# Kernel optimization log

Measured on AMD Instinct MI355X. Metric: run time of the kernel, lower is better.

Reference implementation:

```python
import jax, jax.numpy as jnp
import numpy as np

B, N, CIN, H, W = 4, 1024, 256, 256, 256
R, C = 32, 32            # N = R*C table grid cells
PH, PW, SR = 3, 3, 2     # pool_size, sampling_ratio
D = 512                  # out_channels
SCALE = 0.25             # spatial_scale: image coords -> feature coords
IMG = 1024.0             # image size (H/SCALE)


def setup_inputs() -> dict:
    key = jax.random.key(0)
    ks = jax.random.split(key, 12)
    feats = jax.random.normal(ks[0], (B, CIN, H, W), jnp.float32)
    # build valid quadrilateral boxes (axis-aligned rectangles as 8-pt polys)
    x1 = jax.random.uniform(ks[1], (B, N), minval=0.0, maxval=IMG - 130.0)
    y1 = jax.random.uniform(ks[2], (B, N), minval=0.0, maxval=IMG - 130.0)
    bw = jax.random.uniform(ks[3], (B, N), minval=16.0, maxval=128.0)
    bh = jax.random.uniform(ks[4], (B, N), minval=16.0, maxval=128.0)
    x2, y2 = x1 + bw, y1 + bh
    boxes = jnp.stack([x1, y1, x2, y1, x2, y2, x1, y2], axis=-1)  # [B,N,8]
    img_sizes = jnp.full((B, 2), IMG, jnp.float32)
    IN = CIN * PH * PW
    W1 = jax.random.normal(ks[5], (IN, D), jnp.float32) * 0.02
    b1 = jnp.zeros((D,), jnp.float32)
    W2 = jax.random.normal(ks[6], (D, D), jnp.float32) * 0.02
    b2 = jnp.zeros((D,), jnp.float32)
    Wb = jax.random.normal(ks[7], (4, D), jnp.float32) * 0.02
    bb = jnp.zeros((D,), jnp.float32)
    g1 = jnp.ones((D,), jnp.float32); be1 = jnp.zeros((D,), jnp.float32)
    g2 = jnp.ones((D,), jnp.float32); be2 = jnp.zeros((D,), jnp.float32)
    return {"feats": feats, "boxes": boxes, "img_sizes": img_sizes,
            "W1": W1, "b1": b1, "W2": W2, "b2": b2, "Wb": Wb, "bb": bb,
            "g1": g1, "be1": be1, "g2": g2, "be2": be2}


def _layer_norm(x, g, b, eps=1e-5):
    mu = jnp.mean(x, axis=-1, keepdims=True)
    var = jnp.mean(jnp.square(x - mu), axis=-1, keepdims=True)
    return (x - mu) * jax.lax.rsqrt(var + eps) * g + b


def _bilinear(img, ys, xs):
    # img [Cin,H,W]; ys,xs [P] -> [Cin,P]; torchvision roi_align semantics:
    # zero outside (-1, dim); clamp into [0, dim-1] before interpolation.
    h, w = img.shape[1], img.shape[2]
    valid = (ys > -1.0) & (ys < h) & (xs > -1.0) & (xs < w)
    y = jnp.clip(ys, 0.0, h - 1.0)
    x = jnp.clip(xs, 0.0, w - 1.0)
    y0 = jnp.floor(y).astype(jnp.int32); x0 = jnp.floor(x).astype(jnp.int32)
    y1 = jnp.minimum(y0 + 1, h - 1);     x1 = jnp.minimum(x0 + 1, w - 1)
    ly = y - y0; lx = x - x0; hy = 1.0 - ly; hx = 1.0 - lx
    v = (img[:, y0, x0] * (hy * hx) + img[:, y0, x1] * (hy * lx)
         + img[:, y1, x0] * (ly * hx) + img[:, y1, x1] * (ly * lx))
    return v * valid


def _roi_align_one(img, bb):
    # img [Cin,H,W]; bb [N,4] already in feature coords -> [N,Cin,PH,PW]
    x1, y1, x2, y2 = bb[:, 0], bb[:, 1], bb[:, 2], bb[:, 3]
    rw = jnp.maximum(x2 - x1, 1.0); rh = jnp.maximum(y2 - y1, 1.0)
    binw = rw / PW; binh = rh / PH
    off = (jnp.arange(SR, dtype=jnp.float32) + 0.5) / SR
    gy = (jnp.arange(PH, dtype=jnp.float32)[:, None] + off[None, :]).reshape(-1)  # [PH*SR]
    gx = (jnp.arange(PW, dtype=jnp.float32)[:, None] + off[None, :]).reshape(-1)  # [PW*SR]
    ys = y1[:, None] + gy[None, :] * binh[:, None]  # [N,PH*SR]
    xs = x1[:, None] + gx[None, :] * binw[:, None]  # [N,PW*SR]
    YY = jnp.broadcast_to(ys[:, :, None], (bb.shape[0], PH * SR, PW * SR)).reshape(-1)
    XX = jnp.broadcast_to(xs[:, None, :], (bb.shape[0], PH * SR, PW * SR)).reshape(-1)
    vals = _bilinear(img, YY, XX)  # [Cin, N*PH*SR*PW*SR]
    vals = vals.reshape(CIN, bb.shape[0], PH, SR, PW, SR).mean(axis=(3, 5))
    return vals.transpose(1, 0, 2, 3)


def reference(feats, boxes, img_sizes, W1, b1, W2, b2, Wb, bb, g1, be1, g2, be2):
    # poly2bbox: [B,N,8] -> [B,N,4] axis-aligned boxes
    px, py = boxes[..., 0::2], boxes[..., 1::2]
    bbox = jnp.stack([px.min(-1), py.min(-1), px.max(-1), py.max(-1)], axis=-1)
    # rotated/regular RoIAlign (here bbox path), vmapped over batch images
    pooled = jax.vmap(_roi_align_one)(feats, bbox * SCALE)     # [B,N,Cin,PH,PW]
    flat = pooled.reshape(B, N, CIN * PH * PW)
    lines_feat = jax.nn.relu(flat @ W1 + b1) @ W2 + b2          # [B,N,D]
    # bbox positional embedding (coords normalized by image size)
    denom = jnp.concatenate([img_sizes, img_sizes], axis=-1)[:, None, :]  # [B,1,4] (w,h,w,h)
    pos = _layer_norm(bbox / denom @ Wb + bb, g1, be1)
    out = _layer_norm(lines_feat + pos, g2, be2)                # [B,N,D]
    # align_cells_feat: pack cells into grid [B,D,R,C] (uniform grid -> no pad)
    aligned = out.transpose(0, 2, 1).reshape(B, D, R, C)
    masks = jnp.ones((B, R, C), jnp.float32)
    return aligned, masks
```

## Files before the change

kernel.cpp:

```cpp
#include <hip/hip_runtime.h>
#include <hip/hip_bf16.h>
#include <cstdint>
#include <cstddef>

#define B_    4
#define N_    1024
#define CIN_  256
#define HW_   256
#define D_    512
#define INK_  2304
#define BN_   4096

typedef __attribute__((ext_vector_type(8))) short bf16x8;
typedef __attribute__((ext_vector_type(4))) float f32x4;
typedef __attribute__((ext_vector_type(4))) unsigned short us4;

#define AS1(p) ((const __attribute__((address_space(1))) void*)(p))
#define AS3(p) ((__attribute__((address_space(3))) void*)(p))

__device__ __forceinline__ unsigned short f2bf(float f) {
    union { float f; unsigned u; } v; v.f = f;
    unsigned r = v.u + 0x7fffu + ((v.u >> 16) & 1u);
    return (unsigned short)(r >> 16);
}

template <typename OutT>
__global__ __launch_bounds__(256) void k_t64(
    const float* __restrict__ src, OutT* __restrict__ dst,
    int Mrows, int Ncols, size_t sBatch, size_t dBatch)
{
    constexpr int PAD = (sizeof(OutT) == 2) ? 66 : 67;
    __shared__ OutT tile[64][PAD];
    const int n0 = blockIdx.x * 64;
    const int m0 = blockIdx.y * 64;
    const float* s = src + (size_t)blockIdx.z * sBatch;
    OutT* d = dst + (size_t)blockIdx.z * dBatch;
    const int t  = threadIdx.x;
    const int rr = t >> 4;
    const int cc = t & 15;

    #pragma unroll
    for (int i = 0; i < 4; ++i) {
        int row = i * 16 + rr;
        float4 v = *(const float4*)(s + (size_t)(m0 + row) * Ncols + n0 + cc * 4);
        if constexpr (sizeof(OutT) == 2) {
            tile[row][cc * 4 + 0] = f2bf(v.x);
            tile[row][cc * 4 + 1] = f2bf(v.y);
            tile[row][cc * 4 + 2] = f2bf(v.z);
            tile[row][cc * 4 + 3] = f2bf(v.w);
        } else {
            tile[row][cc * 4 + 0] = v.x;
            tile[row][cc * 4 + 1] = v.y;
            tile[row][cc * 4 + 2] = v.z;
            tile[row][cc * 4 + 3] = v.w;
        }
    }
    __syncthreads();
    #pragma unroll
    for (int i = 0; i < 4; ++i) {
        int p = i * 16 + rr;
        OutT v0 = tile[cc * 4 + 0][p];
        OutT v1 = tile[cc * 4 + 1][p];
        OutT v2 = tile[cc * 4 + 2][p];
        OutT v3 = tile[cc * 4 + 3][p];
        OutT* dp = d + (size_t)(n0 + p) * Mrows + m0 + cc * 4;
        if constexpr (sizeof(OutT) == 2) {
            *(us4*)dp = (us4){(unsigned short)v0, (unsigned short)v1,
                              (unsigned short)v2, (unsigned short)v3};
        } else {
            *(float4*)dp = make_float4(v0, v1, v2, v3);
        }
    }
}

__global__ __launch_bounds__(256) void k_roi3(
    const unsigned short* __restrict__ featsT, const float* __restrict__ boxes,
    unsigned short* __restrict__ flat)
{
    __shared__ int   so[4][36][4];
    __shared__ float sw[4][36][4];
    const int t = threadIdx.x;

    if (t < 144) {
        const int mbx = t / 36, s = t - mbx * 36;
        const int mbn = blockIdx.x * 4 + mbx;
        const float* bx = boxes + (size_t)mbn * 8;
        float xmn = fminf(fminf(bx[0], bx[2]), fminf(bx[4], bx[6]));
        float xmx = fmaxf(fmaxf(bx[0], bx[2]), fmaxf(bx[4], bx[6]));
        float ymn = fminf(fminf(bx[1], bx[3]), fminf(bx[5], bx[7]));
        float ymx = fmaxf(fmaxf(bx[1], bx[3]), fmaxf(bx[5], bx[7]));
        float sx1 = xmn * 0.25f, sy1 = ymn * 0.25f;
        float sx2 = xmx * 0.25f, sy2 = ymx * 0.25f;
        float rw = fmaxf(sx2 - sx1, 1.0f), rh = fmaxf(sy2 - sy1, 1.0f);
        float binw = rw * (1.0f / 3.0f), binh = rh * (1.0f / 3.0f);
        int row = s / 6, col = s % 6;
        float y = sy1 + (row * 0.5f + 0.25f) * binh;
        float x = sx1 + (col * 0.5f + 0.25f) * binw;
        float valid = (y > -1.0f && y < 256.0f && x > -1.0f && x < 256.0f) ? 1.0f : 0.0f;
        y = fminf(fmaxf(y, 0.0f), 255.0f);
        x = fminf(fmaxf(x, 0.0f), 255.0f);
        int y0 = (int)floorf(y), x0 = (int)floorf(x);
        int y1 = min(y0 + 1, 255), x1 = min(x0 + 1, 255);
        float ly = y - (float)y0, lx = x - (float)x0;
        float hy = 1.0f - ly, hx = 1.0f - lx;
        float m = 0.25f * valid;
        so[mbx][s][0] = y0 * HW_ + x0;  so[mbx][s][1] = y0 * HW_ + x1;
        so[mbx][s][2] = y1 * HW_ + x0;  so[mbx][s][3] = y1 * HW_ + x1;
        sw[mbx][s][0] = hy * hx * m;    sw[mbx][s][1] = hy * lx * m;
        sw[mbx][s][2] = ly * hx * m;    sw[mbx][s][3] = ly * lx * m;
    }
    __syncthreads();

    const int bxi = t >> 6;
    const int tid = t & 63;
    const int bn  = blockIdx.x * 4 + bxi;
    const int b   = bn >> 10;
    const uint2* basep = (const uint2*)featsT + (size_t)b * (65536ull * 64ull) + tid;

    float a0[9] = {0,0,0,0,0,0,0,0,0};
    float a1[9] = {0,0,0,0,0,0,0,0,0};
    float a2[9] = {0,0,0,0,0,0,0,0,0};
    float a3[9] = {0,0,0,0,0,0,0,0,0};
    #pragma unroll
    for (int j = 0; j < 36; ++j) {
        const int bin = ((j / 6) >> 1) * 3 + ((j % 6) >> 1);
        #pragma unroll
        for (int p = 0; p < 4; ++p) {
            float wgt = sw[bxi][j][p];
            uint2 u = basep[(size_t)so[bxi][j][p] << 6];
            a0[bin] += wgt * __uint_as_float(u.x << 16);
            a1[bin] += wgt * __uint_as_float(u.x & 0xffff0000u);
            a2[bin] += wgt * __uint_as_float(u.y << 16);
            a3[bin] += wgt * __uint_as_float(u.y & 0xffff0000u);
        }
    }

    unsigned short tmp[36];
    #pragma unroll
    for (int k = 0; k < 9; ++k) {
        tmp[k] = f2bf(a0[k]); tmp[9 + k] = f2bf(a1[k]);
        tmp[18 + k] = f2bf(a2[k]); tmp[27 + k] = f2bf(a3[k]);
    }
    unsigned* dst = (unsigned*)(flat + (size_t)bn * INK_ + tid * 36);
    #pragma unroll
    for (int k = 0; k < 18; ++k)
        dst[k] = (unsigned)tmp[2 * k] | ((unsigned)tmp[2 * k + 1] << 16);
}

template <int K, bool RELU_BF16OUT>
__global__ __launch_bounds__(256) void k_gemmB(
    const unsigned short* __restrict__ A,
    const unsigned short* __restrict__ Bt,
    const float* __restrict__ bias,
    unsigned short* __restrict__ Cbf,
    float* __restrict__ Cf)
{
    __shared__ __align__(16) unsigned short As[2][128 * 32];
    __shared__ __align__(16) unsigned short Bs[2][64 * 32];

    const int t = threadIdx.x;
    const int w = t >> 6;
    const int lane = t & 63;
    const int lane16 = lane & 15;
    const int q = lane >> 4;
    const int m0 = blockIdx.x * 128;
    const int n0 = blockIdx.y * 64;

    const int r4 = lane >> 2, c4 = lane & 3;
    const unsigned short* gA0 = A + (size_t)(m0 + w * 16 + r4) * K + c4 * 8;
    const unsigned short* gA1 = gA0 + (size_t)64 * K;
    const unsigned short* gB  = Bt + (size_t)(n0 + w * 16 + r4) * K + c4 * 8;

    f32x4 acc[2][4] = {};

    __builtin_amdgcn_global_load_lds(AS1(gA0), AS3(&As[0][(w * 16) * 32]), 16, 0, 0);
    __builtin_amdgcn_global_load_lds(AS1(gA1), AS3(&As[0][(64 + w * 16) * 32]), 16, 0, 0);
    __builtin_amdgcn_global_load_lds(AS1(gB ), AS3(&Bs[0][(w * 16) * 32]), 16, 0, 0);
    gA0 += 32; gA1 += 32; gB += 32;

    int cur = 0;
    for (int k0 = 0; k0 < K; k0 += 32) {
        __syncthreads();
        if (k0 + 32 < K) {
            __builtin_amdgcn_global_load_lds(AS1(gA0), AS3(&As[cur ^ 1][(w * 16) * 32]), 16, 0, 0);
            __builtin_amdgcn_global_load_lds(AS1(gA1), AS3(&As[cur ^ 1][(64 + w * 16) * 32]), 16, 0, 0);
            __builtin_amdgcn_global_load_lds(AS1(gB ), AS3(&Bs[cur ^ 1][(w * 16) * 32]), 16, 0, 0);
            gA0 += 32; gA1 += 32; gB += 32;
        }
        bf16x8 a0 = *(const bf16x8*)&As[cur][(w * 32 + lane16) * 32 + q * 8];
        bf16x8 a1 = *(const bf16x8*)&As[cur][(w * 32 + 16 + lane16) * 32 + q * 8];
        #pragma unroll
        for (int nt = 0; nt < 4; ++nt) {
            bf16x8 bv = *(const bf16x8*)&Bs[cur][(nt * 16 + lane16) * 32 + q * 8];
            acc[0][nt] = __builtin_amdgcn_mfma_f32_16x16x32_bf16(a0, bv, acc[0][nt], 0, 0, 0);
            acc[1][nt] = __builtin_amdgcn_mfma_f32_16x16x32_bf16(a1, bv, acc[1][nt], 0, 0, 0);
        }
        cur ^= 1;
    }

    #pragma unroll
    for (int nt = 0; nt < 4; ++nt) {
        int col = n0 + nt * 16 + lane16;
        float bs = bias[col];
        #pragma unroll
        for (int mg = 0; mg < 2; ++mg) {
            #pragma unroll
            for (int r = 0; r < 4; ++r) {
                int row = m0 + w * 32 + mg * 16 + q * 4 + r;
                float v = acc[mg][nt][r] + bs;
                if constexpr (RELU_BF16OUT) {
                    v = fmaxf(v, 0.0f);
                    Cbf[(size_t)row * D_ + col] = f2bf(v);
                } else {
                    Cf[(size_t)row * D_ + col] = v;
                }
            }
        }
    }
}

__global__ __launch_bounds__(256) void k_convert(
    const float* __restrict__ W1, const float* __restrict__ W2,
    unsigned short* __restrict__ W1t, unsigned short* __restrict__ W2t)
{
    int i = blockIdx.x * 256 + threadIdx.x;
    const int n1 = INK_ * D_;
    if (i < n1) {
        int n = i / INK_, k = i % INK_;
        W1t[i] = f2bf(W1[(size_t)k * D_ + n]);
    } else {
        int j = i - n1;
        if (j < D_ * D_) {
            int n = j / D_, k = j % D_;
            W2t[j] = f2bf(W2[(size_t)k * D_ + n]);
        }
    }
}

__global__ __launch_bounds__(256) void k_roi(
    const float* __restrict__ feats, const float* __restrict__ boxes,
    unsigned short* __restrict__ flat)
{
    __shared__ int   so[36][4];
    __shared__ float sw[36][4];
    const int bn = blockIdx.x;
    const int b  = bn >> 10;
    const int t  = threadIdx.x;

    if (t < 36) {
        const float* bx = boxes + (size_t)bn * 8;
        float xmn = fminf(fminf(bx[0], bx[2]), fminf(bx[4], bx[6]));
        float xmx = fmaxf(fmaxf(bx[0], bx[2]), fmaxf(bx[4], bx[6]));
        float ymn = fminf(fminf(bx[1], bx[3]), fminf(bx[5], bx[7]));
        float ymx = fmaxf(fmaxf(bx[1], bx[3]), fmaxf(bx[5], bx[7]));
        float sx1 = xmn * 0.25f, sy1 = ymn * 0.25f;
        float sx2 = xmx * 0.25f, sy2 = ymx * 0.25f;
        float rw = fmaxf(sx2 - sx1, 1.0f), rh = fmaxf(sy2 - sy1, 1.0f);
        float binw = rw * (1.0f / 3.0f), binh = rh * (1.0f / 3.0f);
        int row = t / 6, col = t % 6;
        float y = sy1 + (row * 0.5f + 0.25f) * binh;
        float x = sx1 + (col * 0.5f + 0.25f) * binw;
        float valid = (y > -1.0f && y < 256.0f && x > -1.0f && x < 256.0f) ? 1.0f : 0.0f;
        y = fminf(fmaxf(y, 0.0f), 255.0f);
        x = fminf(fmaxf(x, 0.0f), 255.0f);
        int y0 = (int)floorf(y), x0 = (int)floorf(x);
        int y1 = min(y0 + 1, 255), x1 = min(x0 + 1, 255);
        float ly = y - (float)y0, lx = x - (float)x0;
        float hy = 1.0f - ly, hx = 1.0f - lx;
        float m = 0.25f * valid;
        so[t][0] = y0 * HW_ + x0;  so[t][1] = y0 * HW_ + x1;
        so[t][2] = y1 * HW_ + x0;  so[t][3] = y1 * HW_ + x1;
        sw[t][0] = hy * hx * m;    sw[t][1] = hy * lx * m;
        sw[t][2] = ly * hx * m;    sw[t][3] = ly * lx * m;
    }
    __syncthreads();

    const float* base = feats + ((size_t)(b * CIN_ + t) << 16);
    float acc[9] = {0.f,0.f,0.f,0.f,0.f,0.f,0.f,0.f,0.f};
    #pragma unroll
    for (int j = 0; j < 36; ++j) {
        const int bin = ((j / 6) >> 1) * 3 + ((j % 6) >> 1);
        float v = sw[j][0] * base[so[j][0]] + sw[j][1] * base[so[j][1]]
                + sw[j][2] * base[so[j][2]] + sw[j][3] * base[so[j][3]];
        acc[bin] += v;
    }
    unsigned short* dst = flat + (size_t)bn * INK_ + t * 9;
    #pragma unroll
    for (int k = 0; k < 9; ++k) dst[k] = f2bf(acc[k]);
}

template <int K, bool RELU_BF16OUT>
__global__ __launch_bounds__(256) void k_gemm(
    const unsigned short* __restrict__ A,
    const unsigned short* __restrict__ Bt,
    const float* __restrict__ bias,
    unsigned short* __restrict__ Cbf,
    float* __restrict__ Cf)
{
    __shared__ __align__(16) unsigned short Asl[64 * 40];
    __shared__ __align__(16) unsigned short Bsl[64 * 40];

    const int t  = threadIdx.x;
    const int m0 = blockIdx.x * 64;
    const int n0 = blockIdx.y * 64;
    const int w  = t >> 6;
    const int l  = t & 63;
    const int lane16 = l & 15;
    const int q  = l >> 4;

    f32x4 acc[4] = {};

    const int srow = t >> 2;
    const int sch  = t & 3;
    const unsigned short* ga = A  + (size_t)(m0 + srow) * K + sch * 8;
    const unsigned short* gb = Bt + (size_t)(n0 + srow) * K + sch * 8;
    unsigned short* la = &Asl[srow * 40 + sch * 8];
    unsigned short* lb = &Bsl[srow * 40 + sch * 8];

    for (int k0 = 0; k0 < K; k0 += 32) {
        __syncthreads();
        *(bf16x8*)la = *(const bf16x8*)(ga + k0);
        *(bf16x8*)lb = *(const bf16x8*)(gb + k0);
        __syncthreads();
        bf16x8 af = *(const bf16x8*)&Asl[(w * 16 + lane16) * 40 + q * 8];
        #pragma unroll
        for (int nt = 0; nt < 4; ++nt) {
            bf16x8 bfv = *(const bf16x8*)&Bsl[(nt * 16 + lane16) * 40 + q * 8];
            acc[nt] = __builtin_amdgcn_mfma_f32_16x16x32_bf16(af, bfv, acc[nt], 0, 0, 0);
        }
    }

    #pragma unroll
    for (int nt = 0; nt < 4; ++nt) {
        int col = n0 + nt * 16 + lane16;
        float bs = bias[col];
        #pragma unroll
        for (int r = 0; r < 4; ++r) {
            int rowg = m0 + w * 16 + q * 4 + r;
            float v = acc[nt][r] + bs;
            if constexpr (RELU_BF16OUT) {
                v = fmaxf(v, 0.0f);
                Cbf[(size_t)rowg * D_ + col] = f2bf(v);
            } else {
                Cf[(size_t)rowg * D_ + col] = v;
            }
        }
    }
}

__device__ __forceinline__ void breduce2(float& a, float& b, float* red, int t) {
    #pragma unroll
    for (int off = 32; off > 0; off >>= 1) {
        a += __shfl_down(a, off);
        b += __shfl_down(b, off);
    }
    int w = t >> 6;
    if ((t & 63) == 0) { red[w] = a; red[4 + w] = b; }
    __syncthreads();
    a = red[0] + red[1] + red[2] + red[3];
    b = red[4] + red[5] + red[6] + red[7];
    __syncthreads();
}

template <bool DIRECT>
__global__ __launch_bounds__(256) void k_tail(
    const float* __restrict__ lines, const float* __restrict__ boxes,
    const float* __restrict__ img_sizes,
    const float* __restrict__ Wb,  const float* __restrict__ bbv,
    const float* __restrict__ g1,  const float* __restrict__ be1,
    const float* __restrict__ g2,  const float* __restrict__ be2,
    float* __restrict__ out)
{
    __shared__ float red[8];
    const int row = blockIdx.x;
    const int b = row >> 10, n = row & 1023;
    const int t = threadIdx.x;

    const float* bx = boxes + (size_t)row * 8;
    float xmn = fminf(fminf(bx[0], bx[2]), fminf(bx[4], bx[6]));
    float xmx = fmaxf(fmaxf(bx[0], bx[2]), fmaxf(bx[4], bx[6]));
    float ymn = fminf(fminf(bx[1], bx[3]), fminf(bx[5], bx[7]));
    float ymx = fmaxf(fmaxf(bx[1], bx[3]), fmaxf(bx[5], bx[7]));
    float s0 = img_sizes[b * 2], s1 = img_sizes[b * 2 + 1];
    float q0 = xmn / s0, q1 = ymn / s1, q2 = xmx / s0, q3 = ymx / s1;

    float tv[2], sv[2];
    float sum = 0.f, sumsq = 0.f;
    #pragma unroll
    for (int i = 0; i < 2; ++i) {
        int d = t + i * 256;
        float v = q0 * Wb[d] + q1 * Wb[512 + d] + q2 * Wb[1024 + d] + q3 * Wb[1536 + d] + bbv[d];
        tv[i] = v; sum += v; sumsq += v * v;
    }
    breduce2(sum, sumsq, red, t);
    float mu = sum * (1.0f / 512.0f);
    float var = sumsq * (1.0f / 512.0f) - mu * mu;
    float rs = rsqrtf(var + 1e-5f);

    sum = 0.f; sumsq = 0.f;
    #pragma unroll
    for (int i = 0; i < 2; ++i) {
        int d = t + i * 256;
        float p = (tv[i] - mu) * rs * g1[d] + be1[d];
        float s = lines[(size_t)row * D_ + d] + p;
        sv[i] = s; sum += s; sumsq += s * s;
    }
    breduce2(sum, sumsq, red, t);
    float mu2 = sum * (1.0f / 512.0f);
    float var2 = sumsq * (1.0f / 512.0f) - mu2 * mu2;
    float rs2 = rsqrtf(var2 + 1e-5f);

    #pragma unroll
    for (int i = 0; i < 2; ++i) {
        int d = t + i * 256;
        float o = (sv[i] - mu2) * rs2 * g2[d] + be2[d];
        if constexpr (DIRECT)
            out[(size_t)b * (D_ * N_) + (size_t)d * N_ + n] = o;
        else
            out[(size_t)row * D_ + d] = o;
    }
}

__global__ __launch_bounds__(256) void k_mask(float* __restrict__ out) {
    int i = blockIdx.x * 256 + threadIdx.x;
    if (i < B_ * 32 * 32) out[(size_t)B_ * D_ * N_ + i] = 1.0f;
}

extern "C" void kernel_launch(void* const* d_in, const int* in_sizes, int n_in,
                              void* d_out, int out_size, void* d_ws, size_t ws_size,
                              hipStream_t stream)
{
    const float* feats = (const float*)d_in[0];
    const float* boxes = (const float*)d_in[1];
    const float* img   = (const float*)d_in[2];
    const float* W1    = (const float*)d_in[3];
    const float* b1    = (const float*)d_in[4];
    const float* W2    = (const float*)d_in[5];
    const float* b2    = (const float*)d_in[6];
    const float* Wb    = (const float*)d_in[7];
    const float* bbv   = (const float*)d_in[8];
    const float* g1    = (const float*)d_in[9];
    const float* be1   = (const float*)d_in[10];
    const float* g2    = (const float*)d_in[11];
    const float* be2   = (const float*)d_in[12];
    float* out = (float*)d_out;
    char* ws = (char*)d_ws;

    const size_t OFF_FEATST = 0;
    const size_t OFF_W1T    = 134217728;
    const size_t OFF_W2T    = 136577024;
    const size_t OFF_FLAT   = 137101312;
    const size_t OFF_ACT    = 155975680;
    const size_t OFF_LINES  = 160169984;
    const size_t OFF_OROW   = 168558592;
    const size_t NEED       = 176947200;

    if (ws_size >= NEED) {
        unsigned short* featsT = (unsigned short*)(ws + OFF_FEATST);
        unsigned short* W1t    = (unsigned short*)(ws + OFF_W1T);
        unsigned short* W2t    = (unsigned short*)(ws + OFF_W2T);
        unsigned short* flat   = (unsigned short*)(ws + OFF_FLAT);
        unsigned short* act    = (unsigned short*)(ws + OFF_ACT);
        float*          lines  = (float*)(ws + OFF_LINES);
        float*          orow   = (float*)(ws + OFF_OROW);

        k_t64<unsigned short><<<dim3(HW_*HW_/64, CIN_/64, B_), 256, 0, stream>>>(
            feats, featsT, CIN_, HW_*HW_, (size_t)CIN_*HW_*HW_, (size_t)CIN_*HW_*HW_);
        k_t64<unsigned short><<<dim3(D_/64, INK_/64, 1), 256, 0, stream>>>(
            W1, W1t, INK_, D_, 0, 0);
        k_t64<unsigned short><<<dim3(D_/64, D_/64, 1), 256, 0, stream>>>(
            W2, W2t, D_, D_, 0, 0);

        k_roi3<<<BN_/4, 256, 0, stream>>>(featsT, boxes, flat);

        dim3 gg(32, 8);
        k_gemmB<INK_, true ><<<gg, 256, 0, stream>>>(flat, W1t, b1, act, nullptr);
        k_gemmB<D_,   false><<<gg, 256, 0, stream>>>(act,  W2t, b2, nullptr, lines);

        k_tail<false><<<BN_, 256, 0, stream>>>(lines, boxes, img, Wb, bbv, g1, be1, g2, be2, orow);
        k_t64<float><<<dim3(D_/64, N_/64, B_), 256, 0, stream>>>(
            orow, out, N_, D_, (size_t)N_*D_, (size_t)D_*N_);
        k_mask<<<16, 256, 0, stream>>>(out);
    } else {
        unsigned short* W1t  = (unsigned short*)(ws);
        unsigned short* W2t  = (unsigned short*)(ws + 2359296);
        unsigned short* flat = (unsigned short*)(ws + 2883584);
        unsigned short* act  = (unsigned short*)(ws + 21757952);
        float*          lines= (float*)(ws + 25952256);

        const int convTotal = INK_ * D_ + D_ * D_;
        k_convert<<<(convTotal + 255) / 256, 256, 0, stream>>>(W1, W2, W1t, W2t);
        k_roi<<<BN_, 256, 0, stream>>>(feats, boxes, flat);
        dim3 gg(64, 8);
        k_gemm<INK_, true ><<<gg, 256, 0, stream>>>(flat, W1t, b1, act, nullptr);
        k_gemm<D_,   false><<<gg, 256, 0, stream>>>(act,  W2t, b2, nullptr, lines);
        k_tail<true><<<BN_, 256, 0, stream>>>(lines, boxes, img, Wb, bbv, g1, be1, g2, be2, out);
        k_mask<<<16, 256, 0, stream>>>(out);
    }
}
```

Baseline: 506.4 us.

## Fuse second GEMM, positional layernorms, transpose and mask into one kernel

Result: no change. 506.3 us (-0.0%).

```diff
diff --git a/kernel.cpp b/kernel.cpp
--- a/kernel.cpp
+++ b/kernel.cpp
@@ -219,6 +219,129 @@
     }
 }
 
+__global__ __launch_bounds__(256) void k_fuse2(
+    const unsigned short* __restrict__ act,
+    const unsigned short* __restrict__ W2t,
+    const float* __restrict__ b2,
+    const float* __restrict__ boxes,
+    const float* __restrict__ img_sizes,
+    const float* __restrict__ Wb,  const float* __restrict__ bbv,
+    const float* __restrict__ g1,  const float* __restrict__ be1,
+    const float* __restrict__ g2,  const float* __restrict__ be2,
+    float* __restrict__ out)
+{
+    __shared__ __align__(16) unsigned short Bs[2][512 * 32];
+    float* S2 = (float*)&Bs[0][0];
+
+    const int t = threadIdx.x;
+    const int w = t >> 6, l = t & 63;
+    const int lane16 = l & 15, q = l >> 4;
+    const int m0 = blockIdx.x * 16;
+    const int b  = m0 >> 10;
+
+    const unsigned short* gB = W2t + (size_t)(t >> 2) * D_ + (t & 3) * 8;
+    #pragma unroll
+    for (int i = 0; i < 8; ++i)
+        __builtin_amdgcn_global_load_lds(AS1(gB + (size_t)i * 64 * D_),
+            AS3(&Bs[0][(t >> 2) * 32 + (t & 3) * 8 + i * 2048]), 16, 0, 0);
+
+    f32x4 acc[8] = {};
+    const unsigned short* gA = act + (size_t)(m0 + lane16) * D_ + q * 8;
+
+    int cur = 0;
+    for (int k0 = 0; k0 < D_; k0 += 32) {
+        __syncthreads();
+        bf16x8 av = *(const bf16x8*)(gA + k0);
+        if (k0 + 32 < D_) {
+            #pragma unroll
+            for (int i = 0; i < 8; ++i)
+                __builtin_amdgcn_global_load_lds(AS1(gB + k0 + 32 + (size_t)i * 64 * D_),
+                    AS3(&Bs[cur ^ 1][(t >> 2) * 32 + (t & 3) * 8 + i * 2048]), 16, 0, 0);
+        }
+        #pragma unroll
+        for (int nt = 0; nt < 8; ++nt) {
+            bf16x8 bv = *(const bf16x8*)&Bs[cur][(w * 128 + nt * 16 + lane16) * 32 + q * 8];
+            acc[nt] = __builtin_amdgcn_mfma_f32_16x16x32_bf16(av, bv, acc[nt], 0, 0, 0);
+        }
+        cur ^= 1;
+    }
+    __syncthreads();
+
+    #pragma unroll
+    for (int nt = 0; nt < 8; ++nt) {
+        int col = w * 128 + nt * 16 + lane16;
+        float bs = b2[col];
+        #pragma unroll
+        for (int r = 0; r < 4; ++r)
+            S2[(q * 4 + r) * D_ + col] = acc[nt][r] + bs;
+    }
+    __syncthreads();
+
+    const float si0 = img_sizes[b * 2], si1 = img_sizes[b * 2 + 1];
+    #pragma unroll 1
+    for (int j = 0; j < 4; ++j) {
+        const int rho = w * 4 + j;
+        const float* bx = boxes + (size_t)(m0 + rho) * 8;
+        float xmn = fminf(fminf(bx[0], bx[2]), fminf(bx[4], bx[6]));
+        float xmx = fmaxf(fmaxf(bx[0], bx[2]), fmaxf(bx[4], bx[6]));
+        float ymn = fminf(fminf(bx[1], bx[3]), fminf(bx[5], bx[7]));
+        float ymx = fmaxf(fmaxf(bx[1], bx[3]), fmaxf(bx[5], bx[7]));
+        float q0 = xmn / si0, q1 = ymn / si1, q2 = xmx / si0, q3 = ymx / si1;
+
+        float tp[8], su = 0.f, sq = 0.f;
+        #pragma unroll
+        for (int i = 0; i < 8; ++i) {
+            int d = i * 64 + l;
+            float v = q0 * Wb[d] + q1 * Wb[512 + d] + q2 * Wb[1024 + d]
+                    + q3 * Wb[1536 + d] + bbv[d];
+            tp[i] = v; su += v; sq += v * v;
+        }
+        #pragma unroll
+        for (int off = 32; off > 0; off >>= 1) {
+            su += __shfl_xor(su, off); sq += __shfl_xor(sq, off);
+        }
+        float mu = su * (1.0f / 512.0f);
+        float rs = rsqrtf(sq * (1.0f / 512.0f) - mu * mu + 1e-5f);
+
+        float sv[8]; su = 0.f; sq = 0.f;
+        #pragma unroll
+        for (int i = 0; i < 8; ++i) {
+            int d = i * 64 + l;
+            float p = (tp[i] - mu) * rs * g1[d] + be1[d];
+            float s = S2[rho * D_ + d] + p;
+            sv[i] = s; su += s; sq += s * s;
+        }
+        #pragma unroll
+        for (int off = 32; off > 0; off >>= 1) {
+            su += __shfl_xor(su, off); sq += __shfl_xor(sq, off);
+        }
+        float mu2 = su * (1.0f / 512.0f);
+        float rs2 = rsqrtf(sq * (1.0f / 512.0f) - mu2 * mu2 + 1e-5f);
+
+        #pragma unroll
+        for (int i = 0; i < 8; ++i) {
+            int d = i * 64 + l;
+            S2[rho * D_ + d] = (sv[i] - mu2) * rs2 * g2[d] + be2[d];
+        }
+    }
+    __syncthreads();
+
+    const int nb = m0 & 1023;
+    float* ob = out + (size_t)b * (D_ * N_) + nb;
+    const int dd = t >> 2, part = t & 3;
+    #pragma unroll
+    for (int i = 0; i < 8; ++i) {
+        int d = i * 64 + dd;
+        float4 v;
+        v.x = S2[(part * 4 + 0) * D_ + d];
+        v.y = S2[(part * 4 + 1) * D_ + d];
+        v.z = S2[(part * 4 + 2) * D_ + d];
+        v.w = S2[(part * 4 + 3) * D_ + d];
+        *(float4*)(ob + (size_t)d * N_ + part * 4) = v;
+    }
+    if (t < 16) out[(size_t)B_ * D_ * N_ + m0 + t] = 1.0f;
+}
+
 __global__ __launch_bounds__(256) void k_convert(
     const float* __restrict__ W1, const float* __restrict__ W2,
     unsigned short* __restrict__ W1t, unsigned short* __restrict__ W2t)
@@ -362,7 +485,6 @@
     __syncthreads();
 }
 
-template <bool DIRECT>
 __global__ __launch_bounds__(256) void k_tail(
     const float* __restrict__ lines, const float* __restrict__ boxes,
     const float* __restrict__ img_sizes,
@@ -414,10 +536,7 @@
     for (int i = 0; i < 2; ++i) {
         int d = t + i * 256;
         float o = (sv[i] - mu2) * rs2 * g2[d] + be2[d];
-        if constexpr (DIRECT)
-            out[(size_t)b * (D_ * N_) + (size_t)d * N_ + n] = o;
-        else
-            out[(size_t)row * D_ + d] = o;
+        out[(size_t)b * (D_ * N_) + (size_t)d * N_ + n] = o;
     }
 }
 
@@ -451,9 +570,7 @@
     const size_t OFF_W2T    = 136577024;
     const size_t OFF_FLAT   = 137101312;
     const size_t OFF_ACT    = 155975680;
-    const size_t OFF_LINES  = 160169984;
-    const size_t OFF_OROW   = 168558592;
-    const size_t NEED       = 176947200;
+    const size_t NEED       = 160169984;
 
     if (ws_size >= NEED) {
         unsigned short* featsT = (unsigned short*)(ws + OFF_FEATST);
@@ -461,8 +578,6 @@
         unsigned short* W2t    = (unsigned short*)(ws + OFF_W2T);
         unsigned short* flat   = (unsigned short*)(ws + OFF_FLAT);
         unsigned short* act    = (unsigned short*)(ws + OFF_ACT);
-        float*          lines  = (float*)(ws + OFF_LINES);
-        float*          orow   = (float*)(ws + OFF_OROW);
 
         k_t64<unsigned short><<<dim3(HW_*HW_/64, CIN_/64, B_), 256, 0, stream>>>(
             feats, featsT, CIN_, HW_*HW_, (size_t)CIN_*HW_*HW_, (size_t)CIN_*HW_*HW_);
@@ -474,13 +589,10 @@
         k_roi3<<<BN_/4, 256, 0, stream>>>(featsT, boxes, flat);
 
         dim3 gg(32, 8);
-        k_gemmB<INK_, true ><<<gg, 256, 0, stream>>>(flat, W1t, b1, act, nullptr);
-        k_gemmB<D_,   false><<<gg, 256, 0, stream>>>(act,  W2t, b2, nullptr, lines);
-
-        k_tail<false><<<BN_, 256, 0, stream>>>(lines, boxes, img, Wb, bbv, g1, be1, g2, be2, orow);
-        k_t64<float><<<dim3(D_/64, N_/64, B_), 256, 0, stream>>>(
-            orow, out, N_, D_, (size_t)N_*D_, (size_t)D_*N_);
-        k_mask<<<16, 256, 0, stream>>>(out);
+        k_gemmB<INK_, true><<<gg, 256, 0, stream>>>(flat, W1t, b1, act, nullptr);
+
+        k_fuse2<<<BN_/16, 256, 0, stream>>>(act, W2t, b2, boxes, img,
+                                            Wb, bbv, g1, be1, g2, be2, out);
     } else {
         unsigned short* W1t  = (unsigned short*)(ws);
         unsigned short* W2t  = (unsigned short*)(ws + 2359296);
@@ -494,7 +606,7 @@
         dim3 gg(64, 8);
         k_gemm<INK_, true ><<<gg, 256, 0, stream>>>(flat, W1t, b1, act, nullptr);
         k_gemm<D_,   false><<<gg, 256, 0, stream>>>(act,  W2t, b2, nullptr, lines);
-        k_tail<true><<<BN_, 256, 0, stream>>>(lines, boxes, img, Wb, bbv, g1, be1, g2, be2, out);
+        k_tail<<<BN_, 256, 0, stream>>>(lines, boxes, img, Wb, bbv, g1, be1, g2, be2, out);
         k_mask<<<16, 256, 0, stream>>>(out);
     }
 }
```
